# Kernel tuning notes

Measured on AMD Instinct MI355X. Metric: run time of the kernel, lower is better.

The kernel has to match this reference:

```python
import jax, jax.numpy as jnp
import numpy as np

BETA = 1.0
GAMMA = 0.25


def setup_inputs() -> dict:
    key = jax.random.key(0)
    ks = jax.random.split(key, 8)
    N, D_in, D_h, D_z = 65536, 1024, 512, 256
    s = lambda fan_in: 1.0 / np.sqrt(fan_in)
    return {
        "x": jax.random.normal(ks[0], (N, D_in), jnp.float32),
        "eW1": jax.random.normal(ks[1], (D_in, D_h), jnp.float32) * s(D_in),
        "eb1": jnp.zeros((D_h,), jnp.float32),
        "eW2": jax.random.normal(ks[2], (D_h, D_z), jnp.float32) * s(D_h),
        "eb2": jnp.zeros((D_z,), jnp.float32),
        "dW1": jax.random.normal(ks[3], (D_z, D_h), jnp.float32) * s(D_z),
        "db1": jnp.zeros((D_h,), jnp.float32),
        "dW2": jax.random.normal(ks[4], (D_h, D_in), jnp.float32) * s(D_h),
        "db2": jnp.zeros((D_in,), jnp.float32),
        "C0": jax.random.normal(ks[5], (1024, D_z), jnp.float32),
        "C1": jax.random.normal(ks[6], (512, D_z), jnp.float32),
        "C2": jax.random.normal(ks[7], (256, D_z), jnp.float32),
    }


def _nearest_idx(r, C):
    # argmin of squared euclidean distance == argmin of cdist(p=2)
    r = jax.lax.stop_gradient(r)
    d2 = jnp.sum(r * r, -1, keepdims=True) - 2.0 * (r @ C.T) + jnp.sum(C * C, -1)
    return jnp.argmin(d2, axis=-1)


def reference(x, eW1, eb1, eW2, eb2, dW1, db1, dW2, db2, C0, C1, C2):
    sg = jax.lax.stop_gradient
    # encoder: Linear -> GELU (exact) -> Linear
    z = jax.nn.gelu(x @ eW1 + eb1, approximate=False) @ eW2 + eb2
    residual = z
    output = jnp.zeros_like(z)
    losses = []
    for C in (C0, C1, C2):
        idx = _nearest_idx(residual, sg(C))
        q = C[idx]                                    # [N, 256] gather
        z2c = jnp.mean((residual - sg(q)) ** 2)       # commit input to code
        c2z = jnp.mean((sg(residual) - q) ** 2)       # move code to input
        losses.append(BETA * c2z + GAMMA * z2c)
        output = output + q
        residual = residual - q
    # straight-through: z + sg(zq) - sg(z)
    h = z + sg(output) - sg(z)
    out = jax.nn.gelu(h @ dW1 + db1, approximate=False) @ dW2 + db2
    recon_loss = jnp.mean((out - x) ** 2)
    return jnp.stack([recon_loss] + losses)  # [4]: recon, commit0, commit1, commit2
```

## Files before the change

kernel.cpp:

```cpp
#include <hip/hip_runtime.h>
#include <cstddef>


typedef __attribute__((ext_vector_type(8))) __bf16 bf16x8;
typedef __attribute__((ext_vector_type(4))) float f32x4;
typedef unsigned short u16;

__device__ __forceinline__ u16 f2bf(float f) {
    unsigned u = __float_as_uint(f);
    u += 0x7fffu + ((u >> 16) & 1u);
    return (u16)(u >> 16);
}
__device__ __forceinline__ float bf2f(u16 b) {
    return __uint_as_float((unsigned)b << 16);
}
__device__ __forceinline__ float gelu_exact(float v) {
    return 0.5f * v * (1.0f + erff(v * 0.7071067811865475f));
}
__device__ __forceinline__ void gload16(const void* g, void* l) {
    __builtin_amdgcn_global_load_lds(
        (const __attribute__((address_space(1))) void*)g,
        (__attribute__((address_space(3))) void*)l, 16, 0, 0);
}
__device__ __forceinline__ f32x4 mfma_bf16(bf16x8 a, bf16x8 b, f32x4 c) {
    return __builtin_amdgcn_mfma_f32_16x16x32_bf16(a, b, c, 0, 0, 0);
}

__global__ __launch_bounds__(256)
void prep_x(const float* __restrict__ x, u16* __restrict__ xbf)
{
    const size_t total = (size_t)65536 * 1024;
    const size_t step  = (size_t)gridDim.x * 256 * 8;
    for (size_t i = ((size_t)blockIdx.x * 256 + threadIdx.x) * 8; i < total; i += step) {
        float4 v0 = *(const float4*)&x[i];
        float4 v1 = *(const float4*)&x[i + 4];
        uint4 o;
        o.x = (unsigned)f2bf(v0.x) | ((unsigned)f2bf(v0.y) << 16);
        o.y = (unsigned)f2bf(v0.z) | ((unsigned)f2bf(v0.w) << 16);
        o.z = (unsigned)f2bf(v1.x) | ((unsigned)f2bf(v1.y) << 16);
        o.w = (unsigned)f2bf(v1.z) | ((unsigned)f2bf(v1.w) << 16);
        *(uint4*)&xbf[i] = o;
    }
}

__global__ __launch_bounds__(256)
void prep_weights(const float* __restrict__ eW1, const float* __restrict__ eW2,
                  const float* __restrict__ dW1, const float* __restrict__ dW2,
                  u16* __restrict__ eW1t, u16* __restrict__ eW2t,
                  u16* __restrict__ dW1t, u16* __restrict__ dW2t)
{
    const int b = blockIdx.x, t = threadIdx.x;
    if (b < 2048) {
        int e = b * 256 + t;
        int n = e >> 10, k = e & 1023;
        eW1t[e] = f2bf(eW1[(size_t)k * 512 + n]);
    } else if (b < 2560) {
        int e = (b - 2048) * 256 + t;
        int n = e >> 9, k = e & 511;
        eW2t[e] = f2bf(eW2[(size_t)k * 256 + n]);
    } else if (b < 3072) {
        int e = (b - 2560) * 256 + t;
        int n = e >> 8, k = e & 255;
        dW1t[e] = f2bf(dW1[(size_t)k * 512 + n]);
    } else {
        int e = (b - 3072) * 256 + t;
        int n = e >> 9, k = e & 511;
        dW2t[e] = f2bf(dW2[(size_t)k * 1024 + n]);
    }
}

__global__ __launch_bounds__(256)
void cb_prep(const float* __restrict__ C0, const float* __restrict__ C1,
             const float* __restrict__ C2, u16* __restrict__ Cbf,
             float* __restrict__ cnorm)
{
    __shared__ float red[256];
    const int code = blockIdx.x, t = threadIdx.x;
    const float* C;
    int local;
    if (code < 1024)      { C = C0; local = code; }
    else if (code < 1536) { C = C1; local = code - 1024; }
    else                  { C = C2; local = code - 1536; }
    const float v = C[(size_t)local * 256 + t];
    Cbf[(size_t)code * 256 + t] = f2bf(v);
    red[t] = v * v;
    __syncthreads();
    for (int s = 128; s; s >>= 1) { if (t < s) red[t] += red[t + s]; __syncthreads(); }
    if (t == 0) cnorm[code] = red[0];
}

template <int EPI>
__global__ __launch_bounds__(512, 2)
void gemm_mfma(const u16* __restrict__ A, const u16* __restrict__ Bt,
               const float* __restrict__ bias, u16* __restrict__ Obf,
               float* __restrict__ Of, const u16* __restrict__ Xbf,
               float* __restrict__ lossOut, int N, int K, int ntn,
               float lossScale)
{
    __shared__ __align__(16) u16 SA[2][2][8192];
    __shared__ __align__(16) u16 SB[2][2][8192];

    const int nwg = gridDim.x;
    const int bid = blockIdx.x;
    const int wg  = (bid & 7) * (nwg >> 3) + (bid >> 3);
    const int brow = (wg / ntn) * 256;
    const int bcol = (wg % ntn) * 256;

    const int t    = threadIdx.x;
    const int lane = t & 63;
    const int wid  = t >> 6;
    const int wrow = (wid >> 2) * 128;
    const int wcol = (wid & 3) * 64;
    const int lrow = lane & 15, g = lane >> 4;

    const int nt = K >> 6;

    f32x4 acc[8][4];
#pragma unroll
    for (int m = 0; m < 8; ++m)
#pragma unroll
        for (int n = 0; n < 4; ++n) acc[m][n] = (f32x4)0.f;

    auto stage_half = [&](const u16* __restrict__ src, int row0, int Ts,
                          int kh, char* region) {
#pragma unroll
        for (int it = 0; it < 2; ++it) {
            const int d  = (it * 512 + t) * 16;
            const int R  = d >> 6;
            const int cs = ((d >> 4) & 3) ^ ((R >> 1) & 3);
            gload16(&src[(size_t)(row0 + R) * K + Ts * 64 + kh * 32 + cs * 8],
                    region + d);
        }
    };

    stage_half(A,  brow, 0, 0, (char*)&SA[0][0][0]);
    stage_half(Bt, bcol, 0, 0, (char*)&SB[0][0][0]);
    stage_half(A,  brow, 0, 1, (char*)&SA[0][1][0]);
    stage_half(Bt, bcol, 0, 1, (char*)&SB[0][1][0]);
    stage_half(A,  brow, 1, 0, (char*)&SA[1][0][0]);
    stage_half(Bt, bcol, 1, 0, (char*)&SB[1][0][0]);
    asm volatile("s_waitcnt vmcnt(8)" ::: "memory");
    __builtin_amdgcn_s_barrier();

    bf16x8 bfr[4];

#define PHASE(MH, KK, DO_B, STAGE_CODE)                                        \
    {                                                                          \
        bf16x8 a_[4];                                                          \
        _Pragma("unroll")                                                      \
        for (int mi = 0; mi < 4; ++mi) {                                       \
            const int R = wrow + ((MH) * 4 + mi) * 16 + lrow;                  \
            a_[mi] = *(const bf16x8*)((const char*)&SA[d][KK][0]               \
                      + R * 64 + ((g ^ ((R >> 1) & 3)) << 4));                 \
        }                                                                      \
        if (DO_B) {                                                            \
            _Pragma("unroll")                                                  \
            for (int n = 0; n < 4; ++n) {                                      \
                const int R = wcol + n * 16 + lrow;                            \
                bfr[n] = *(const bf16x8*)((const char*)&SB[d][KK][0]           \
                          + R * 64 + ((g ^ ((R >> 1) & 3)) << 4));             \
            }                                                                  \
        }                                                                      \
        STAGE_CODE;                                                            \
        if (T >= nt - 2) asm volatile("s_waitcnt vmcnt(0)" ::: "memory");      \
        else             asm volatile("s_waitcnt vmcnt(8)" ::: "memory");      \
        __builtin_amdgcn_s_barrier();                                          \
        __builtin_amdgcn_s_setprio(1);                                         \
        _Pragma("unroll")                                                      \
        for (int mi = 0; mi < 4; ++mi)                                         \
            _Pragma("unroll")                                                  \
            for (int n = 0; n < 4; ++n)                                        \
                acc[(MH) * 4 + mi][n] =                                        \
                    mfma_bf16(a_[mi], bfr[n], acc[(MH) * 4 + mi][n]);          \
        __builtin_amdgcn_s_setprio(0);                                         \
        __builtin_amdgcn_s_barrier();                                          \
    }

    for (int T = 0; T < nt; ++T) {
        const int d = T & 1;
        PHASE(0, 0, 1,
              if (T + 1 < nt) stage_half(A, brow, T + 1, 1,
                                         (char*)&SA[(T + 1) & 1][1][0]));
        PHASE(1, 0, 0,
              if (T + 1 < nt) stage_half(Bt, bcol, T + 1, 1,
                                         (char*)&SB[(T + 1) & 1][1][0]));
        PHASE(0, 1, 1,
              if (T + 2 < nt) stage_half(A, brow, T + 2, 0,
                                         (char*)&SA[T & 1][0][0]));
        PHASE(1, 1, 0,
              if (T + 2 < nt) stage_half(Bt, bcol, T + 2, 0,
                                         (char*)&SB[T & 1][0][0]));
    }
#undef PHASE

    int   colN[4];
    float bn[4];
#pragma unroll
    for (int n = 0; n < 4; ++n) {
        colN[n] = bcol + wcol + n * 16 + lrow;
        bn[n]   = bias[colN[n]];
    }

    if (EPI == 0) {
#pragma unroll
        for (int m = 0; m < 8; ++m) {
            const int rowb = brow + wrow + m * 16 + (lane >> 4) * 4;
#pragma unroll
            for (int n = 0; n < 4; ++n)
#pragma unroll
                for (int j = 0; j < 4; ++j)
                    Obf[(size_t)(rowb + j) * N + colN[n]] =
                        f2bf(gelu_exact(acc[m][n][j] + bn[n]));
        }
    } else if (EPI == 1) {
#pragma unroll
        for (int m = 0; m < 8; ++m) {
            const int rowb = brow + wrow + m * 16 + (lane >> 4) * 4;
#pragma unroll
            for (int n = 0; n < 4; ++n)
#pragma unroll
                for (int j = 0; j < 4; ++j)
                    Of[(size_t)(rowb + j) * N + colN[n]] = acc[m][n][j] + bn[n];
        }
    } else {
        float partial = 0.f;
#pragma unroll
        for (int m = 0; m < 8; ++m) {
            const int rowb = brow + wrow + m * 16 + (lane >> 4) * 4;
#pragma unroll
            for (int n = 0; n < 4; ++n)
#pragma unroll
                for (int j = 0; j < 4; ++j) {
                    const float o = acc[m][n][j] + bn[n];
                    const float d = o - bf2f(Xbf[(size_t)(rowb + j) * N + colN[n]]);
                    partial = fmaf(d, d, partial);
                }
        }
        __syncthreads();
        float* red = (float*)&SA[0][0][0];
        red[t] = partial;
        __syncthreads();
        for (int s = 256; s; s >>= 1) { if (t < s) red[t] += red[t + s]; __syncthreads(); }
        if (t == 0) atomicAdd(lossOut, red[0] * lossScale);
    }
}

__global__ __launch_bounds__(512, 4)
void vq_mfma(const float* __restrict__ Z, const u16* __restrict__ Cbf,
             const float* __restrict__ cnorm,
             const float* __restrict__ C0, const float* __restrict__ C1,
             const float* __restrict__ C2,
             u16* __restrict__ ZQ, float* __restrict__ lossOut)
{
    __shared__ __align__(16) u16 Rb[64][264];
    __shared__ __align__(16) u16 Cs[2][32 * 256];
    __shared__ float redv[64][2];
    __shared__ int   redi[64][2];
    __shared__ int   idxs[3][64];
    __shared__ float lred[8];

    const int t    = threadIdx.x;
    const int lane = t & 63;
    const int wid  = t >> 6;
    const int rg   = wid & 3;
    const int cg   = wid >> 2;
    const int lrow = lane & 15, g = lane >> 4;
    const int col  = t & 255;
    const int rh   = t >> 8;
    const int brow = blockIdx.x * 64;

    float R[32];
#pragma unroll
    for (int r = 0; r < 32; ++r)
        R[r] = Z[(size_t)(brow + rh * 32 + r) * 256 + col];

    const float* Cf[3]  = {C0, C1, C2};
    const int ncodes[3] = {1024, 512, 256};
    const int coff[3]   = {0, 1024, 1536};
    const float lscale  = 1.25f / (65536.0f * 256.0f);

    for (int stage = 0; stage < 3; ++stage) {
        const u16*   Cb  = Cbf + (size_t)coff[stage] * 256;
        const float* cns = cnorm + coff[stage];
        const int ntile  = ncodes[stage] >> 5;

        auto stageC = [&](int tile, int buf) {
#pragma unroll
            for (int it = 0; it < 2; ++it) {
                const int d   = (it * 512 + t) * 16;
                const int row = d >> 9;
                const int kb  = d & 511;
                const int kbs = kb ^ ((row & 7) << 4);
                gload16(&Cb[(size_t)(tile * 32 + row) * 256 + (kbs >> 1)],
                        (char*)&Cs[buf][0] + d);
            }
        };

        stageC(0, 0);
#pragma unroll
        for (int r = 0; r < 32; ++r) Rb[rh * 32 + r][col] = f2bf(R[r]);
        __syncthreads();

        bf16x8 a[8];
#pragma unroll
        for (int ks = 0; ks < 8; ++ks)
            a[ks] = *(const bf16x8*)&Rb[rg * 16 + lrow][ks * 32 + g * 8];

        float best[4]; int bidx[4];
#pragma unroll
        for (int j = 0; j < 4; ++j) { best[j] = 3.0e38f; bidx[j] = 0; }

        const int cr = cg * 16 + lrow;

        int buf = 0;
#pragma unroll 1
        for (int tile = 0; tile < ntile; ++tile) {
            if (tile + 1 < ntile) stageC(tile + 1, buf ^ 1);
            const int   code = tile * 32 + cr;
            const float cn   = cns[code];
            f32x4 acc = (f32x4)0.f;
#pragma unroll
            for (int ks = 0; ks < 8; ++ks) {
                const int kb = (ks * 64 + g * 16) ^ ((cr & 7) << 4);
                bf16x8 b = *(const bf16x8*)((const char*)&Cs[buf][0]
                             + cr * 512 + kb);
                acc = mfma_bf16(a[ks], b, acc);
            }
#pragma unroll
            for (int j = 0; j < 4; ++j) {
                const float s = fmaf(-2.0f, acc[j], cn);
                if (s < best[j]) { best[j] = s; bidx[j] = code; }
            }
            __syncthreads();
            buf ^= 1;
        }

#pragma unroll
        for (int j = 0; j < 4; ++j) {
            float v = best[j]; int i = bidx[j];
#pragma unroll
            for (int d = 1; d < 16; d <<= 1) {
                const float ov = __shfl_xor(v, d);
                const int   oi = __shfl_xor(i, d);
                if (ov < v || (ov == v && oi < i)) { v = ov; i = oi; }
            }
            if (lrow == 0) {
                redv[rg * 16 + g * 4 + j][cg] = v;
                redi[rg * 16 + g * 4 + j][cg] = i;
            }
        }
        __syncthreads();
        if (t < 64) {
            float v = redv[t][0]; int i = redi[t][0];
            const float ov = redv[t][1]; const int oi = redi[t][1];
            if (ov < v || (ov == v && oi < i)) { v = ov; i = oi; }
            idxs[stage][t] = i;
        }
        __syncthreads();

        const float* Cfs = Cf[stage];
        float partial = 0.f;
#pragma unroll
        for (int r = 0; r < 32; ++r) {
            const float q  = Cfs[(size_t)idxs[stage][rh * 32 + r] * 256 + col];
            const float rn = R[r] - q;
            R[r] = rn;
            partial = fmaf(rn, rn, partial);
        }
#pragma unroll
        for (int d = 32; d; d >>= 1) partial += __shfl_down(partial, d);
        if (lane == 0) lred[wid] = partial;
        __syncthreads();
        if (t == 0) {
            float s = 0.f;
#pragma unroll
            for (int w2 = 0; w2 < 8; ++w2) s += lred[w2];
            atomicAdd(&lossOut[1 + stage], s * lscale);
        }
        __syncthreads();
    }

#pragma unroll
    for (int r = 0; r < 32; ++r) {
        const int row = rh * 32 + r;
        const float zq = C0[(size_t)idxs[0][row] * 256 + col]
                       + C1[(size_t)idxs[1][row] * 256 + col]
                       + C2[(size_t)idxs[2][row] * 256 + col];
        ZQ[(size_t)(brow + row) * 256 + col] = f2bf(zq);
    }
}

extern "C" void kernel_launch(void* const* d_in, const int* in_sizes, int n_in,
                              void* d_out, int out_size, void* d_ws, size_t ws_size,
                              hipStream_t stream)
{
    const float* x   = (const float*)d_in[0];
    const float* eW1 = (const float*)d_in[1];
    const float* eb1 = (const float*)d_in[2];
    const float* eW2 = (const float*)d_in[3];
    const float* eb2 = (const float*)d_in[4];
    const float* dW1 = (const float*)d_in[5];
    const float* db1 = (const float*)d_in[6];
    const float* dW2 = (const float*)d_in[7];
    const float* db2 = (const float*)d_in[8];
    const float* C0  = (const float*)d_in[9];
    const float* C1  = (const float*)d_in[10];
    const float* C2  = (const float*)d_in[11];
    float* out = (float*)d_out;

    char* w = (char*)d_ws;
    u16*   H1   = (u16*)(w);
    float* Zf   = (float*)(w + ((size_t)64 << 20));
    u16*   ZQ   = (u16*)(w + ((size_t)128 << 20));
    u16*   H2   = (u16*)(w + ((size_t)160 << 20));
    u16*   xbf  = (u16*)(w + ((size_t)230 << 20));
    u16*   eW1t = (u16*)(w + ((size_t)224 << 20));
    u16*   eW2t = (u16*)(w + ((size_t)225 << 20));
    u16*   dW1t = (u16*)(w + ((size_t)226 << 20));
    u16*   dW2t = (u16*)(w + ((size_t)227 << 20));
    u16*   Cbf  = (u16*)(w + ((size_t)228 << 20));
    float* cn   = (float*)(w + ((size_t)229 << 20));

    hipMemsetAsync(d_out, 0, 4 * sizeof(float), stream);

    prep_x<<<4096, 256, 0, stream>>>(x, xbf);
    prep_weights<<<5120, 256, 0, stream>>>(eW1, eW2, dW1, dW2, eW1t, eW2t, dW1t, dW2t);
    cb_prep<<<1792, 256, 0, stream>>>(C0, C1, C2, Cbf, cn);

    gemm_mfma<0><<<512, 512, 0, stream>>>(
        xbf, eW1t, eb1, H1, nullptr, nullptr, nullptr, 512, 1024, 2, 0.f);
    gemm_mfma<1><<<256, 512, 0, stream>>>(
        H1, eW2t, eb2, nullptr, Zf, nullptr, nullptr, 256, 512, 1, 0.f);
    vq_mfma<<<1024, 512, 0, stream>>>(Zf, Cbf, cn, C0, C1, C2, ZQ, out);
    gemm_mfma<0><<<512, 512, 0, stream>>>(
        ZQ, dW1t, db1, H2, nullptr, nullptr, nullptr, 512, 256, 2, 0.f);
    gemm_mfma<2><<<1024, 512, 0, stream>>>(
        H2, dW2t, db2, nullptr, nullptr, xbf, out, 1024, 512, 4,
        1.0f / (65536.0f * 1024.0f));
}
```

Baseline: 541.3 us.

## Triple-buffer VQ codebook tiles with 64-code tiles and 2x16 row blocks per wave

The VQ nearest-code kernel now stages 64-code tiles into a three-deep LDS ring, prefetching two tiles ahead. It synchronises with explicit vmcnt waits plus a barrier instead of a trailing __syncthreads. Each wave now computes two 16-row blocks against one shared B fragment, reusing each LDS codebook read across two MFMAs, and the argmin reduction now spans four code groups. LDS use grows to about 130KB and launch bounds drop to 2 blocks per CU, trading occupancy for fewer barriers and more reuse.

```diff
diff --git a/kernel.cpp b/kernel.cpp
--- a/kernel.cpp
+++ b/kernel.cpp
@@ -245,7 +245,7 @@
     }
 }
 
-__global__ __launch_bounds__(512, 4)
+__global__ __launch_bounds__(512, 2)
 void vq_mfma(const float* __restrict__ Z, const u16* __restrict__ Cbf,
              const float* __restrict__ cnorm,
              const float* __restrict__ C0, const float* __restrict__ C1,
@@ -253,17 +253,17 @@
              u16* __restrict__ ZQ, float* __restrict__ lossOut)
 {
     __shared__ __align__(16) u16 Rb[64][264];
-    __shared__ __align__(16) u16 Cs[2][32 * 256];
-    __shared__ float redv[64][2];
-    __shared__ int   redi[64][2];
+    __shared__ __align__(16) u16 Cs[3][64 * 256];
+    __shared__ float redv[64][4];
+    __shared__ int   redi[64][4];
     __shared__ int   idxs[3][64];
     __shared__ float lred[8];
 
     const int t    = threadIdx.x;
     const int lane = t & 63;
     const int wid  = t >> 6;
-    const int rg   = wid & 3;
-    const int cg   = wid >> 2;
+    const int rh2  = wid >> 2;
+    const int cq   = wid & 3;
     const int lrow = lane & 15, g = lane >> 4;
     const int col  = t & 255;
     const int rh   = t >> 8;
@@ -279,81 +279,97 @@
     const int coff[3]   = {0, 1024, 1536};
     const float lscale  = 1.25f / (65536.0f * 256.0f);
 
+    const int cr2 = cq * 16 + lrow;
+
     for (int stage = 0; stage < 3; ++stage) {
         const u16*   Cb  = Cbf + (size_t)coff[stage] * 256;
         const float* cns = cnorm + coff[stage];
-        const int ntile  = ncodes[stage] >> 5;
+        const int ntile  = ncodes[stage] >> 6;
 
         auto stageC = [&](int tile, int buf) {
 #pragma unroll
-            for (int it = 0; it < 2; ++it) {
+            for (int it = 0; it < 4; ++it) {
                 const int d   = (it * 512 + t) * 16;
                 const int row = d >> 9;
                 const int kb  = d & 511;
                 const int kbs = kb ^ ((row & 7) << 4);
-                gload16(&Cb[(size_t)(tile * 32 + row) * 256 + (kbs >> 1)],
+                gload16(&Cb[(size_t)(tile * 64 + row) * 256 + (kbs >> 1)],
                         (char*)&Cs[buf][0] + d);
             }
         };
 
         stageC(0, 0);
+        if (ntile > 1) stageC(1, 1);
 #pragma unroll
         for (int r = 0; r < 32; ++r) Rb[rh * 32 + r][col] = f2bf(R[r]);
         __syncthreads();
 
-        bf16x8 a[8];
-#pragma unroll
-        for (int ks = 0; ks < 8; ++ks)
-            a[ks] = *(const bf16x8*)&Rb[rg * 16 + lrow][ks * 32 + g * 8];
-
-        float best[4]; int bidx[4];
-#pragma unroll
-        for (int j = 0; j < 4; ++j) { best[j] = 3.0e38f; bidx[j] = 0; }
-
-        const int cr = cg * 16 + lrow;
-
-        int buf = 0;
+        bf16x8 a0[8], a1[8];
+#pragma unroll
+        for (int ks = 0; ks < 8; ++ks) {
+            a0[ks] = *(const bf16x8*)&Rb[rh2 * 32 + lrow][ks * 32 + g * 8];
+            a1[ks] = *(const bf16x8*)&Rb[rh2 * 32 + 16 + lrow][ks * 32 + g * 8];
+        }
+
+        float best[2][4]; int bidx[2][4];
+#pragma unroll
+        for (int m = 0; m < 2; ++m)
+#pragma unroll
+            for (int j = 0; j < 4; ++j) { best[m][j] = 3.0e38f; bidx[m][j] = 0; }
+
 #pragma unroll 1
         for (int tile = 0; tile < ntile; ++tile) {
-            if (tile + 1 < ntile) stageC(tile + 1, buf ^ 1);
-            const int   code = tile * 32 + cr;
+            if (tile + 1 < ntile) asm volatile("s_waitcnt vmcnt(4)" ::: "memory");
+            else                  asm volatile("s_waitcnt vmcnt(0)" ::: "memory");
+            __builtin_amdgcn_s_barrier();
+            if (tile + 2 < ntile) stageC(tile + 2, (tile + 2) % 3);
+
+            const int   buf  = tile % 3;
+            const int   code = tile * 64 + cr2;
             const float cn   = cns[code];
-            f32x4 acc = (f32x4)0.f;
+            f32x4 acc0 = (f32x4)0.f, acc1 = (f32x4)0.f;
 #pragma unroll
             for (int ks = 0; ks < 8; ++ks) {
-                const int kb = (ks * 64 + g * 16) ^ ((cr & 7) << 4);
+                const int kb = (ks * 64 + g * 16) ^ ((cr2 & 7) << 4);
                 bf16x8 b = *(const bf16x8*)((const char*)&Cs[buf][0]
-                             + cr * 512 + kb);
-                acc = mfma_bf16(a[ks], b, acc);
+                             + cr2 * 512 + kb);
+                acc0 = mfma_bf16(a0[ks], b, acc0);
+                acc1 = mfma_bf16(a1[ks], b, acc1);
             }
 #pragma unroll
             for (int j = 0; j < 4; ++j) {
-                const float s = fmaf(-2.0f, acc[j], cn);
-                if (s < best[j]) { best[j] = s; bidx[j] = code; }
+                const float s0 = fmaf(-2.0f, acc0[j], cn);
+                if (s0 < best[0][j]) { best[0][j] = s0; bidx[0][j] = code; }
+                const float s1 = fmaf(-2.0f, acc1[j], cn);
+                if (s1 < best[1][j]) { best[1][j] = s1; bidx[1][j] = code; }
             }
-            __syncthreads();
-            buf ^= 1;
-        }
-
-#pragma unroll
-        for (int j = 0; j < 4; ++j) {
-            float v = best[j]; int i = bidx[j];
-#pragma unroll
-            for (int d = 1; d < 16; d <<= 1) {
-                const float ov = __shfl_xor(v, d);
-                const int   oi = __shfl_xor(i, d);
+        }
+
+#pragma unroll
+        for (int m = 0; m < 2; ++m)
+#pragma unroll
+            for (int j = 0; j < 4; ++j) {
+                float v = best[m][j]; int i = bidx[m][j];
+#pragma unroll
+                for (int d = 1; d < 16; d <<= 1) {
+                    const float ov = __shfl_xor(v, d);
+                    const int   oi = __shfl_xor(i, d);
+                    if (ov < v || (ov == v && oi < i)) { v = ov; i = oi; }
+                }
+                if (lrow == 0) {
+                    redv[rh2 * 32 + m * 16 + g * 4 + j][cq] = v;
+                    redi[rh2 * 32 + m * 16 + g * 4 + j][cq] = i;
+                }
+            }
+        __syncthreads();
+        if (t < 64) {
+            float v = redv[t][0]; int i = redi[t][0];
+#pragma unroll
+            for (int w2 = 1; w2 < 4; ++w2) {
+                const float ov = redv[t][w2];
+                const int   oi = redi[t][w2];
                 if (ov < v || (ov == v && oi < i)) { v = ov; i = oi; }
             }
-            if (lrow == 0) {
-                redv[rg * 16 + g * 4 + j][cg] = v;
-                redi[rg * 16 + g * 4 + j][cg] = i;
-            }
-        }
-        __syncthreads();
-        if (t < 64) {
-            float v = redv[t][0]; int i = redi[t][0];
-            const float ov = redv[t][1]; const int oi = redi[t][1];
-            if (ov < v || (ov == v && oi < i)) { v = ov; i = oi; }
             idxs[stage][t] = i;
         }
         __syncthreads();
```

Result: slower. 589.0 us (+8.8%).

## Store encoder output as bf16 and deepen VQ codebook pipeline with half-tile staging

Applied to the files above, without the earlier changes.

The encoder's second GEMM now writes z in bf16 instead of fp32, which halves the write and the read-back traffic into the VQ kernel. The VQ kernel splits each 32-code tile into two K-halves and keeps three half-tiles of loads in flight. It uses explicit vmcnt waits and raw barriers instead of a full __syncthreads per tile, and raises wave priority around the MFMAs. The risk is that residuals start from a bf16-rounded z, which changes the loss values and could flip near-tie argmins.

```diff
diff --git a/kernel.cpp b/kernel.cpp
--- a/kernel.cpp
+++ b/kernel.cpp
@@ -222,6 +222,17 @@
                 for (int j = 0; j < 4; ++j)
                     Of[(size_t)(rowb + j) * N + colN[n]] = acc[m][n][j] + bn[n];
         }
+    } else if (EPI == 3) {
+#pragma unroll
+        for (int m = 0; m < 8; ++m) {
+            const int rowb = brow + wrow + m * 16 + (lane >> 4) * 4;
+#pragma unroll
+            for (int n = 0; n < 4; ++n)
+#pragma unroll
+                for (int j = 0; j < 4; ++j)
+                    Obf[(size_t)(rowb + j) * N + colN[n]] =
+                        f2bf(acc[m][n][j] + bn[n]);
+        }
     } else {
         float partial = 0.f;
 #pragma unroll
@@ -246,14 +257,14 @@
 }
 
 __global__ __launch_bounds__(512, 4)
-void vq_mfma(const float* __restrict__ Z, const u16* __restrict__ Cbf,
+void vq_mfma(const u16* __restrict__ Zbf, const u16* __restrict__ Cbf,
              const float* __restrict__ cnorm,
              const float* __restrict__ C0, const float* __restrict__ C1,
              const float* __restrict__ C2,
              u16* __restrict__ ZQ, float* __restrict__ lossOut)
 {
     __shared__ __align__(16) u16 Rb[64][264];
-    __shared__ __align__(16) u16 Cs[2][32 * 256];
+    __shared__ __align__(16) u16 Cs[2][2][32 * 128];
     __shared__ float redv[64][2];
     __shared__ int   redi[64][2];
     __shared__ int   idxs[3][64];
@@ -272,31 +283,34 @@
     float R[32];
 #pragma unroll
     for (int r = 0; r < 32; ++r)
-        R[r] = Z[(size_t)(brow + rh * 32 + r) * 256 + col];
+        R[r] = bf2f(Zbf[(size_t)(brow + rh * 32 + r) * 256 + col]);
 
     const float* Cf[3]  = {C0, C1, C2};
     const int ncodes[3] = {1024, 512, 256};
     const int coff[3]   = {0, 1024, 1536};
     const float lscale  = 1.25f / (65536.0f * 256.0f);
 
+    const int cr = cg * 16 + lrow;
+
     for (int stage = 0; stage < 3; ++stage) {
         const u16*   Cb  = Cbf + (size_t)coff[stage] * 256;
         const float* cns = cnorm + coff[stage];
         const int ntile  = ncodes[stage] >> 5;
-
-        auto stageC = [&](int tile, int buf) {
-#pragma unroll
-            for (int it = 0; it < 2; ++it) {
-                const int d   = (it * 512 + t) * 16;
-                const int row = d >> 9;
-                const int kb  = d & 511;
-                const int kbs = kb ^ ((row & 7) << 4);
-                gload16(&Cb[(size_t)(tile * 32 + row) * 256 + (kbs >> 1)],
-                        (char*)&Cs[buf][0] + d);
-            }
+        const int nh     = ntile * 2;
+
+        auto stageH = [&](int h) {
+            const int tile = h >> 1, kh = h & 1;
+            const int d    = t * 16;
+            const int row  = d >> 8;
+            const int kb   = d & 255;
+            const int kbs  = kb ^ ((row & 7) << 4);
+            gload16(&Cb[(size_t)(tile * 32 + row) * 256 + kh * 128 + (kbs >> 1)],
+                    (char*)&Cs[tile & 1][kh][0] + d);
         };
 
-        stageC(0, 0);
+        stageH(0);
+        stageH(1);
+        if (nh > 2) stageH(2);
 #pragma unroll
         for (int r = 0; r < 32; ++r) Rb[rh * 32 + r][col] = f2bf(R[r]);
         __syncthreads();
@@ -310,29 +324,39 @@
 #pragma unroll
         for (int j = 0; j < 4; ++j) { best[j] = 3.0e38f; bidx[j] = 0; }
 
-        const int cr = cg * 16 + lrow;
-
-        int buf = 0;
+        f32x4 acc = (f32x4)0.f;
 #pragma unroll 1
-        for (int tile = 0; tile < ntile; ++tile) {
-            if (tile + 1 < ntile) stageC(tile + 1, buf ^ 1);
-            const int   code = tile * 32 + cr;
-            const float cn   = cns[code];
-            f32x4 acc = (f32x4)0.f;
-#pragma unroll
-            for (int ks = 0; ks < 8; ++ks) {
-                const int kb = (ks * 64 + g * 16) ^ ((cr & 7) << 4);
-                bf16x8 b = *(const bf16x8*)((const char*)&Cs[buf][0]
-                             + cr * 512 + kb);
-                acc = mfma_bf16(a[ks], b, acc);
+        for (int h = 0; h < nh; ++h) {
+            const int tile = h >> 1, kh = h & 1;
+            const char* Cbuf = (const char*)&Cs[tile & 1][kh][0];
+            bf16x8 b[4];
+#pragma unroll
+            for (int ks2 = 0; ks2 < 4; ++ks2) {
+                const int kb2 = (ks2 * 64 + g * 16) ^ ((cr & 7) << 4);
+                b[ks2] = *(const bf16x8*)(Cbuf + cr * 256 + kb2);
             }
-#pragma unroll
-            for (int j = 0; j < 4; ++j) {
-                const float s = fmaf(-2.0f, acc[j], cn);
-                if (s < best[j]) { best[j] = s; bidx[j] = code; }
+            if (h + 3 < nh) stageH(h + 3);
+            const int newer = nh - (h + 2);
+            if (newer >= 2)      asm volatile("s_waitcnt vmcnt(2)" ::: "memory");
+            else if (newer == 1) asm volatile("s_waitcnt vmcnt(1)" ::: "memory");
+            else                 asm volatile("s_waitcnt vmcnt(0)" ::: "memory");
+            __builtin_amdgcn_s_barrier();
+            __builtin_amdgcn_s_setprio(1);
+#pragma unroll
+            for (int ks2 = 0; ks2 < 4; ++ks2)
+                acc = mfma_bf16(a[kh * 4 + ks2], b[ks2], acc);
+            __builtin_amdgcn_s_setprio(0);
+            if (kh == 1) {
+                const int   code = tile * 32 + cr;
+                const float cn   = cns[code];
+#pragma unroll
+                for (int j = 0; j < 4; ++j) {
+                    const float s = fmaf(-2.0f, acc[j], cn);
+                    if (s < best[j]) { best[j] = s; bidx[j] = code; }
+                }
+                acc = (f32x4)0.f;
             }
-            __syncthreads();
-            buf ^= 1;
+            __builtin_amdgcn_s_barrier();
         }
 
 #pragma unroll
@@ -410,7 +434,7 @@
 
     char* w = (char*)d_ws;
     u16*   H1   = (u16*)(w);
-    float* Zf   = (float*)(w + ((size_t)64 << 20));
+    u16*   Zbf  = (u16*)(w + ((size_t)64 << 20));
     u16*   ZQ   = (u16*)(w + ((size_t)128 << 20));
     u16*   H2   = (u16*)(w + ((size_t)160 << 20));
     u16*   xbf  = (u16*)(w + ((size_t)230 << 20));
@@ -429,9 +453,9 @@
 
     gemm_mfma<0><<<512, 512, 0, stream>>>(
         xbf, eW1t, eb1, H1, nullptr, nullptr, nullptr, 512, 1024, 2, 0.f);
-    gemm_mfma<1><<<256, 512, 0, stream>>>(
-        H1, eW2t, eb2, nullptr, Zf, nullptr, nullptr, 256, 512, 1, 0.f);
-    vq_mfma<<<1024, 512, 0, stream>>>(Zf, Cbf, cn, C0, C1, C2, ZQ, out);
+    gemm_mfma<3><<<256, 512, 0, stream>>>(
+        H1, eW2t, eb2, Zbf, nullptr, nullptr, nullptr, 256, 512, 1, 0.f);
+    vq_mfma<<<1024, 512, 0, stream>>>(Zbf, Cbf, cn, C0, C1, C2, ZQ, out);
     gemm_mfma<0><<<512, 512, 0, stream>>>(
         ZQ, dW1t, db1, H2, nullptr, nullptr, nullptr, 512, 256, 2, 0.f);
     gemm_mfma<2><<<1024, 512, 0, stream>>>(
```

Result: slower. 926.3 us (+71.1%).

## Triple-buffer codebook tiles in VQ kernel and store encoder output as bf16

Applied to the files above, without the earlier changes.

The VQ kernel's codebook staging moves from a double buffer with a full __syncthreads per tile to a three-slot ring in a shared pool. It prefetches two tiles ahead and waits with explicit vmcnt plus a bare s_barrier, and raises wave priority around the MFMA loop. Separately, the encoder's second GEMM gets a new epilogue that writes z as bf16 instead of fp32, halving the VQ kernel's input read. This changes numerics: the residual and the commitment losses are now computed from a bf16-rounded z. LDS use grows to about 65 KB per block, which may lower the number of blocks resident per CU.

```diff
diff --git a/kernel.cpp b/kernel.cpp
--- a/kernel.cpp
+++ b/kernel.cpp
@@ -222,6 +222,17 @@
                 for (int j = 0; j < 4; ++j)
                     Of[(size_t)(rowb + j) * N + colN[n]] = acc[m][n][j] + bn[n];
         }
+    } else if (EPI == 3) {
+#pragma unroll
+        for (int m = 0; m < 8; ++m) {
+            const int rowb = brow + wrow + m * 16 + (lane >> 4) * 4;
+#pragma unroll
+            for (int n = 0; n < 4; ++n)
+#pragma unroll
+                for (int j = 0; j < 4; ++j)
+                    Obf[(size_t)(rowb + j) * N + colN[n]] =
+                        f2bf(acc[m][n][j] + bn[n]);
+        }
     } else {
         float partial = 0.f;
 #pragma unroll
@@ -246,18 +257,19 @@
 }
 
 __global__ __launch_bounds__(512, 4)
-void vq_mfma(const float* __restrict__ Z, const u16* __restrict__ Cbf,
+void vq_mfma(const u16* __restrict__ Zbf, const u16* __restrict__ Cbf,
              const float* __restrict__ cnorm,
              const float* __restrict__ C0, const float* __restrict__ C1,
              const float* __restrict__ C2,
              u16* __restrict__ ZQ, float* __restrict__ lossOut)
 {
-    __shared__ __align__(16) u16 Rb[64][264];
-    __shared__ __align__(16) u16 Cs[2][32 * 256];
+    __shared__ __align__(16) char pool[66560];
     __shared__ float redv[64][2];
     __shared__ int   redi[64][2];
     __shared__ int   idxs[3][64];
     __shared__ float lred[8];
+
+    u16 (*Rb)[264] = (u16 (*)[264])(pool + 32768);
 
     const int t    = threadIdx.x;
     const int lane = t & 63;
@@ -272,19 +284,22 @@
     float R[32];
 #pragma unroll
     for (int r = 0; r < 32; ++r)
-        R[r] = Z[(size_t)(brow + rh * 32 + r) * 256 + col];
+        R[r] = bf2f(Zbf[(size_t)(brow + rh * 32 + r) * 256 + col]);
 
     const float* Cf[3]  = {C0, C1, C2};
     const int ncodes[3] = {1024, 512, 256};
     const int coff[3]   = {0, 1024, 1536};
     const float lscale  = 1.25f / (65536.0f * 256.0f);
 
+    const int cr = cg * 16 + lrow;
+
     for (int stage = 0; stage < 3; ++stage) {
         const u16*   Cb  = Cbf + (size_t)coff[stage] * 256;
         const float* cns = cnorm + coff[stage];
         const int ntile  = ncodes[stage] >> 5;
 
-        auto stageC = [&](int tile, int buf) {
+        auto stageC = [&](int tile) {
+            char* region = pool + (size_t)(tile % 3) * 16384;
 #pragma unroll
             for (int it = 0; it < 2; ++it) {
                 const int d   = (it * 512 + t) * 16;
@@ -292,11 +307,12 @@
                 const int kb  = d & 511;
                 const int kbs = kb ^ ((row & 7) << 4);
                 gload16(&Cb[(size_t)(tile * 32 + row) * 256 + (kbs >> 1)],
-                        (char*)&Cs[buf][0] + d);
+                        region + d);
             }
         };
 
-        stageC(0, 0);
+        stageC(0);
+        if (ntile > 1) stageC(1);
 #pragma unroll
         for (int r = 0; r < 32; ++r) Rb[rh * 32 + r][col] = f2bf(R[r]);
         __syncthreads();
@@ -305,34 +321,38 @@
 #pragma unroll
         for (int ks = 0; ks < 8; ++ks)
             a[ks] = *(const bf16x8*)&Rb[rg * 16 + lrow][ks * 32 + g * 8];
+        __syncthreads();
 
         float best[4]; int bidx[4];
 #pragma unroll
         for (int j = 0; j < 4; ++j) { best[j] = 3.0e38f; bidx[j] = 0; }
 
-        const int cr = cg * 16 + lrow;
-
-        int buf = 0;
 #pragma unroll 1
         for (int tile = 0; tile < ntile; ++tile) {
-            if (tile + 1 < ntile) stageC(tile + 1, buf ^ 1);
+            if (tile >= 1) {
+                if (tile + 1 < ntile) asm volatile("s_waitcnt vmcnt(2)" ::: "memory");
+                else                  asm volatile("s_waitcnt vmcnt(0)" ::: "memory");
+                __builtin_amdgcn_s_barrier();
+            }
+            if (tile + 2 < ntile) stageC(tile + 2);
+
+            const char* Cbuf = pool + (size_t)(tile % 3) * 16384;
             const int   code = tile * 32 + cr;
             const float cn   = cns[code];
             f32x4 acc = (f32x4)0.f;
+            __builtin_amdgcn_s_setprio(1);
 #pragma unroll
             for (int ks = 0; ks < 8; ++ks) {
                 const int kb = (ks * 64 + g * 16) ^ ((cr & 7) << 4);
-                bf16x8 b = *(const bf16x8*)((const char*)&Cs[buf][0]
-                             + cr * 512 + kb);
+                bf16x8 b = *(const bf16x8*)(Cbuf + cr * 512 + kb);
                 acc = mfma_bf16(a[ks], b, acc);
             }
+            __builtin_amdgcn_s_setprio(0);
 #pragma unroll
             for (int j = 0; j < 4; ++j) {
                 const float s = fmaf(-2.0f, acc[j], cn);
                 if (s < best[j]) { best[j] = s; bidx[j] = code; }
             }
-            __syncthreads();
-            buf ^= 1;
         }
 
 #pragma unroll
@@ -410,7 +430,7 @@
 
     char* w = (char*)d_ws;
     u16*   H1   = (u16*)(w);
-    float* Zf   = (float*)(w + ((size_t)64 << 20));
+    u16*   Zbf  = (u16*)(w + ((size_t)64 << 20));
     u16*   ZQ   = (u16*)(w + ((size_t)128 << 20));
     u16*   H2   = (u16*)(w + ((size_t)160 << 20));
     u16*   xbf  = (u16*)(w + ((size_t)230 << 20));
@@ -429,9 +449,9 @@
 
     gemm_mfma<0><<<512, 512, 0, stream>>>(
         xbf, eW1t, eb1, H1, nullptr, nullptr, nullptr, 512, 1024, 2, 0.f);
-    gemm_mfma<1><<<256, 512, 0, stream>>>(
-        H1, eW2t, eb2, nullptr, Zf, nullptr, nullptr, 256, 512, 1, 0.f);
-    vq_mfma<<<1024, 512, 0, stream>>>(Zf, Cbf, cn, C0, C1, C2, ZQ, out);
+    gemm_mfma<3><<<256, 512, 0, stream>>>(
+        H1, eW2t, eb2, Zbf, nullptr, nullptr, nullptr, 256, 512, 1, 0.f);
+    vq_mfma<<<1024, 512, 0, stream>>>(Zbf, Cbf, cn, C0, C1, C2, ZQ, out);
     gemm_mfma<0><<<512, 512, 0, stream>>>(
         ZQ, dW1t, db1, H2, nullptr, nullptr, nullptr, 512, 256, 2, 0.f);
     gemm_mfma<2><<<1024, 512, 0, stream>>>(
```

After: 549.9 us. No clear change (+1.6%).
